# Kernel optimization log

Hardware: AMD Instinct MI355X
Metric: run time of the kernel (lower is better)

The kernel has to match this reference:

```python
import jax, jax.numpy as jnp
import numpy as np

B, S, D, HD = 4, 4096, 1024, 64

def setup_inputs() -> dict:
    key = jax.random.key(0)
    ks = jax.random.split(key, 4)
    scale = 1.0 / np.sqrt(D)
    return {
        "x": jax.random.normal(ks[0], (B, S, D), dtype=jnp.float32),
        "wq": jax.random.normal(ks[1], (HD, D), dtype=jnp.float32) * scale,
        "bq": jnp.zeros((HD,), dtype=jnp.float32),
        "wk": jax.random.normal(ks[2], (HD, D), dtype=jnp.float32) * scale,
        "bk": jnp.zeros((HD,), dtype=jnp.float32),
        "wv": jax.random.normal(ks[3], (HD, D), dtype=jnp.float32) * scale,
        "bv": jnp.zeros((HD,), dtype=jnp.float32),
    }

def reference(x, wq, bq, wk, bk, wv, bv):
    seq_len = x.shape[1]
    head_dim = wq.shape[0]
    # projections: nn.Linear stores weight as [out, in]
    q = jnp.einsum('bsd,hd->bsh', x, wq) + bq  # [B,S,HD]
    k = jnp.einsum('bsd,hd->bsh', x, wk) + bk
    v = jnp.einsum('bsd,hd->bsh', x, wv) + bv
    score = jnp.einsum('bqh,bkh->bqk', q, k) / jnp.sqrt(jnp.float32(head_dim))  # [B,S,S]
    causal = jnp.tril(jnp.ones((seq_len, seq_len), dtype=bool))
    score = jnp.where(causal, score, -jnp.inf)
    attn = jax.nn.softmax(score, axis=-1)
    # dropout p=0.0 -> identity
    out = jnp.einsum('bqk,bkh->bqh', attn, v)  # [B,S,HD]
    return out
```

## Files before the change

### kernel.cpp

```cpp
#include <hip/hip_runtime.h>
#include <math.h>

#define B_   4
#define S_   4096
#define D_   1024
#define HD_  64

#define CK            8
#define CHUNKS_PER_B  288
#define PSTRIDE       68
#define SLOT_F        (64 * PSTRIDE)

typedef float  f32x4  __attribute__((ext_vector_type(4)));
typedef __bf16 bf16x8 __attribute__((ext_vector_type(8)));

static __device__ __forceinline__ unsigned short f2bf(float f) {
    unsigned int u = __float_as_uint(f);
    u += 0x7FFFu + ((u >> 16) & 1u);
    return (unsigned short)(u >> 16);
}

__global__ __launch_bounds__(256) void convert_w(
    const float* __restrict__ wq, const float* __restrict__ wk,
    const float* __restrict__ wv, unsigned short* __restrict__ wbf)
{
    const int col = blockIdx.x;
    const int p = col >> 6, h = col & 63;
    const float* src = (p == 0 ? wq : (p == 1 ? wk : wv)) + (size_t)h * D_;
    const int t = threadIdx.x;
    const float4 v = ((const float4*)src)[t];
    ushort4 o;
    o.x = f2bf(v.x); o.y = f2bf(v.y); o.z = f2bf(v.z); o.w = f2bf(v.w);
    *(ushort4*)&wbf[(size_t)col * D_ + 4 * t] = o;
}

__global__ __launch_bounds__(256) void proj_mfma(
    const float* __restrict__ x, const unsigned short* __restrict__ wbf,
    const float* __restrict__ bq, const float* __restrict__ bk,
    const float* __restrict__ bv,
    unsigned short* __restrict__ qbf, unsigned short* __restrict__ kbf,
    unsigned short* __restrict__ vtb)
{
    __shared__ unsigned short xs[32][72];
    __shared__ unsigned short wsh[96][72];

    const int t = threadIdx.x;
    const int w = t >> 6, lane = t & 63;
    const int n = lane & 15, g = lane >> 4;
    const int koff = 8 * g;
    const int rt = w & 1, cg = w >> 1;
    const size_t row0 = (size_t)blockIdx.x * 32;
    const int colbase = 96 * blockIdx.y;

    f32x4 acc[3];
#pragma unroll
    for (int i = 0; i < 3; ++i) acc[i] = (f32x4)0.f;

    for (int chunk = 0; chunk < 16; ++chunk) {
        const int d0 = chunk * 64;
        __syncthreads();
#pragma unroll
        for (int i = 0; i < 2; ++i) {
            int e = t + i * 256;
            int r = e >> 4, c4 = (e & 15) * 4;
            float4 v = *(const float4*)&x[(row0 + r) * D_ + d0 + c4];
            ushort4 o;
            o.x = f2bf(v.x); o.y = f2bf(v.y); o.z = f2bf(v.z); o.w = f2bf(v.w);
            *(ushort4*)&xs[r][c4] = o;
        }
#pragma unroll
        for (int i = 0; i < 3; ++i) {
            int e = t + i * 256;
            int col = e >> 3, gg = e & 7;
            uint4 v = *(const uint4*)&wbf[(size_t)(colbase + col) * D_ + d0 + 8 * gg];
            *(uint4*)&wsh[col][8 * gg] = v;
        }
        __syncthreads();

#pragma unroll
        for (int ks = 0; ks < 2; ++ks) {
            const int k0 = 32 * ks;
            const bf16x8 a = *(const bf16x8*)&xs[16 * rt + n][k0 + koff];
#pragma unroll
            for (int ci = 0; ci < 3; ++ci) {
                const bf16x8 b = *(const bf16x8*)&wsh[48 * cg + 16 * ci + n][k0 + koff];
                acc[ci] = __builtin_amdgcn_mfma_f32_16x16x32_bf16(a, b, acc[ci], 0, 0, 0);
            }
        }
    }

#pragma unroll
    for (int ci = 0; ci < 3; ++ci) {
        const int gct = 6 * blockIdx.y + 3 * cg + ci;
        const int p = gct >> 2, h0 = (gct & 3) * 16;
        const int h = h0 + n;
        const float bb = (p == 0 ? bq : (p == 1 ? bk : bv))[h];
        if (p == 2) {
            const size_t grow0 = row0 + 16 * rt + 4 * g;
            const int bidx = (int)(grow0 >> 12);
            const int s0 = (int)(grow0 & 4095);
            ushort4 u;
            u.x = f2bf(acc[ci][0] + bb); u.y = f2bf(acc[ci][1] + bb);
            u.z = f2bf(acc[ci][2] + bb); u.w = f2bf(acc[ci][3] + bb);
            *(ushort4*)&vtb[((size_t)bidx * HD_ + h) * S_ + s0] = u;
        } else {
            unsigned short* outp = (p == 0 ? qbf : kbf);
            const float scale = (p == 0) ? 0.125f : 1.0f;
#pragma unroll
            for (int r = 0; r < 4; ++r) {
                const size_t grow = row0 + 16 * rt + 4 * g + r;
                outp[grow * HD_ + h] = f2bf((acc[ci][r] + bb) * scale);
            }
        }
    }
}

__global__ __launch_bounds__(256) void flash_splitk(
    const unsigned short* __restrict__ qg, const unsigned short* __restrict__ kg,
    const unsigned short* __restrict__ vt, float* __restrict__ out,
    float* __restrict__ part)
{
    __shared__ unsigned short qsh[64][72];
    __shared__ unsigned short ksh[64][72];
    __shared__ unsigned short vsh[64][72];
    __shared__ unsigned short psh[4][16][72];

    const int t    = threadIdx.x;
    const int w    = t >> 6;
    const int lane = t & 63;
    const int n    = lane & 15;
    const int g    = lane >> 4;
    const int koff = 8 * g;
    const int b    = blockIdx.y;

    int qi = 0, rem = blockIdx.x;
    while (rem >= ((qi >> 3) + 1)) { rem -= (qi >> 3) + 1; ++qi; }
    const int c   = rem;
    const int kt0 = c * CK;
    const int kt1 = min(qi, kt0 + CK - 1);
    const int nc  = (qi >> 3) + 1;

    const size_t qtile = ((size_t)b * S_ + (size_t)qi * 64) * HD_;

    {
        const uint4* src = (const uint4*)(qg + qtile);
#pragma unroll
        for (int i = 0; i < 2; ++i) {
            int e = t + i * 256;
            int r = e >> 3, gg = e & 7;
            *(uint4*)&qsh[r][8 * gg] = src[e];
        }
    }

    f32x4 o4[4];
#pragma unroll
    for (int i = 0; i < 4; ++i) o4[i] = (f32x4)0.f;
    float m_r = -INFINITY, l_r = 0.f;

    for (int kt = kt0; kt <= kt1; ++kt) {
        const size_t kvbase = ((size_t)b * S_ + (size_t)kt * 64) * HD_;
        __syncthreads();
        {
            const uint4* ksrc = (const uint4*)(kg + kvbase);
#pragma unroll
            for (int i = 0; i < 2; ++i) {
                int e = t + i * 256;
                int r = e >> 3, gg = e & 7;
                *(uint4*)&ksh[r][8 * gg] = ksrc[e];
            }
#pragma unroll
            for (int i = 0; i < 2; ++i) {
                int e = t + i * 256;
                int h = e >> 3, gg = e & 7;
                *(uint4*)&vsh[h][8 * gg] =
                    *(const uint4*)&vt[((size_t)b * HD_ + h) * S_ + kt * 64 + 8 * gg];
            }
        }
        __syncthreads();

        f32x4 sc[4];
#pragma unroll
        for (int mt = 0; mt < 4; ++mt) sc[mt] = (f32x4)0.f;
#pragma unroll
        for (int ks = 0; ks < 2; ++ks) {
            const bf16x8 bq8 = *(const bf16x8*)&qsh[16 * w + n][32 * ks + koff];
#pragma unroll
            for (int mt = 0; mt < 4; ++mt) {
                const bf16x8 ak = *(const bf16x8*)&ksh[16 * mt + n][32 * ks + koff];
                sc[mt] = __builtin_amdgcn_mfma_f32_16x16x32_bf16(ak, bq8, sc[mt], 0, 0, 0);
            }
        }

        if (kt == qi) {
            const int qloc = 16 * w + n;
#pragma unroll
            for (int mt = 0; mt < 4; ++mt)
#pragma unroll
                for (int r = 0; r < 4; ++r) {
                    const int kloc = 16 * mt + 4 * g + r;
                    if (kloc > qloc) sc[mt][r] = -INFINITY;
                }
        }

        float mx = -INFINITY;
#pragma unroll
        for (int mt = 0; mt < 4; ++mt)
#pragma unroll
            for (int r = 0; r < 4; ++r) mx = fmaxf(mx, sc[mt][r]);
        mx = fmaxf(mx, __shfl_xor(mx, 16));
        mx = fmaxf(mx, __shfl_xor(mx, 32));

        const float m_new = fmaxf(m_r, mx);
        const float alpha = __expf(m_r - m_new);
        float psum = 0.f;
#pragma unroll
        for (int mt = 0; mt < 4; ++mt)
#pragma unroll
            for (int r = 0; r < 4; ++r) {
                const float p = __expf(sc[mt][r] - m_new);
                sc[mt][r] = p;
                psum += p;
            }
        psum += __shfl_xor(psum, 16);
        psum += __shfl_xor(psum, 32);
        l_r = l_r * alpha + psum;
        m_r = m_new;

#pragma unroll
        for (int r = 0; r < 4; ++r) {
            const float ar = __shfl(alpha, 4 * g + r);
#pragma unroll
            for (int ht = 0; ht < 4; ++ht) o4[ht][r] *= ar;
        }

#pragma unroll
        for (int mt = 0; mt < 4; ++mt) {
            ushort4 u;
            u.x = f2bf(sc[mt][0]); u.y = f2bf(sc[mt][1]);
            u.z = f2bf(sc[mt][2]); u.w = f2bf(sc[mt][3]);
            *(ushort4*)&psh[w][n][16 * mt + 4 * g] = u;
        }

#pragma unroll
        for (int ks = 0; ks < 2; ++ks) {
            const bf16x8 ap = *(const bf16x8*)&psh[w][n][32 * ks + koff];
#pragma unroll
            for (int ht = 0; ht < 4; ++ht) {
                const bf16x8 bv8 = *(const bf16x8*)&vsh[16 * ht + n][32 * ks + koff];
                o4[ht] = __builtin_amdgcn_mfma_f32_16x16x32_bf16(ap, bv8, o4[ht], 0, 0, 0);
            }
        }
    }

    const size_t qbase = ((size_t)b * S_ + (size_t)qi * 64) * HD_;
    if (nc == 1) {
#pragma unroll
        for (int r = 0; r < 4; ++r) {
            const float lr = __shfl(l_r, 4 * g + r);
            const float inv = 1.f / lr;
            const size_t ob = qbase + (size_t)(16 * w + 4 * g + r) * HD_;
#pragma unroll
            for (int ht = 0; ht < 4; ++ht)
                out[ob + 16 * ht + n] = o4[ht][r] * inv;
        }
    } else {
        const size_t sb = ((size_t)b * CHUNKS_PER_B + blockIdx.x) * SLOT_F;
#pragma unroll
        for (int r = 0; r < 4; ++r) {
            const size_t pb = sb + (size_t)(16 * w + 4 * g + r) * PSTRIDE;
#pragma unroll
            for (int ht = 0; ht < 4; ++ht)
                part[pb + 16 * ht + n] = o4[ht][r];
        }
        if (g == 0) {
            part[sb + (size_t)(16 * w + n) * PSTRIDE + 64] = m_r;
            part[sb + (size_t)(16 * w + n) * PSTRIDE + 65] = l_r;
        }
    }
}

__global__ __launch_bounds__(256) void combine(
    const float* __restrict__ part, float* __restrict__ out)
{
    const int t  = threadIdx.x;
    const int qr = t >> 2, tc = t & 3;
    const int qi = blockIdx.x + CK;
    const int b  = blockIdx.y;
    const int nc = (qi >> 3) + 1;

    int cum = 0;
    for (int j = 0; j < qi; ++j) cum += (j >> 3) + 1;
    const size_t base0 = ((size_t)b * CHUNKS_PER_B + cum) * SLOT_F;

    float M = -INFINITY;
    for (int c0 = 0; c0 < nc; ++c0)
        M = fmaxf(M, part[base0 + (size_t)c0 * SLOT_F + qr * PSTRIDE + 64]);

    float L = 0.f;
    float o[16];
#pragma unroll
    for (int j = 0; j < 16; ++j) o[j] = 0.f;

    for (int c0 = 0; c0 < nc; ++c0) {
        const size_t sb = base0 + (size_t)c0 * SLOT_F + qr * PSTRIDE;
        const float m_c = part[sb + 64];
        const float l_c = part[sb + 65];
        const float w = __expf(m_c - M);
        L += w * l_c;
#pragma unroll
        for (int j = 0; j < 4; ++j) {
            const float4 ov = *(const float4*)&part[sb + tc * 16 + 4 * j];
            o[4 * j + 0] += w * ov.x; o[4 * j + 1] += w * ov.y;
            o[4 * j + 2] += w * ov.z; o[4 * j + 3] += w * ov.w;
        }
    }

    const float inv = 1.f / L;
    const size_t qbase = ((size_t)b * S_ + (size_t)qi * 64) * HD_;
#pragma unroll
    for (int j = 0; j < 4; ++j) {
        float4 r;
        r.x = o[4 * j + 0] * inv; r.y = o[4 * j + 1] * inv;
        r.z = o[4 * j + 2] * inv; r.w = o[4 * j + 3] * inv;
        *(float4*)&out[qbase + 16 * t + 4 * j] = r;
    }
}

extern "C" void kernel_launch(void* const* d_in, const int* in_sizes, int n_in,
                              void* d_out, int out_size, void* d_ws, size_t ws_size,
                              hipStream_t stream)
{
    const float* x  = (const float*)d_in[0];
    const float* wq = (const float*)d_in[1];
    const float* bq = (const float*)d_in[2];
    const float* wk = (const float*)d_in[3];
    const float* bk = (const float*)d_in[4];
    const float* wv = (const float*)d_in[5];
    const float* bv = (const float*)d_in[6];
    float* outp = (float*)d_out;

    const size_t n = (size_t)B_ * S_ * HD_;
    unsigned short* qbf = (unsigned short*)d_ws;
    unsigned short* kbf = qbf + n;
    unsigned short* vtb = kbf + n;
    unsigned short* wbf = vtb + n;
    float* part = (float*)(wbf + (size_t)192 * D_);

    convert_w<<<dim3(192), 256, 0, stream>>>(wq, wk, wv, wbf);
    proj_mfma<<<dim3(B_ * S_ / 32, 2), 256, 0, stream>>>(
        x, wbf, bq, bk, bv, qbf, kbf, vtb);
    flash_splitk<<<dim3(CHUNKS_PER_B, B_), 256, 0, stream>>>(qbf, kbf, vtb, outp, part);
    combine<<<dim3(S_ / 64 - CK, B_), 256, 0, stream>>>(part, outp);
}
```

Baseline: 174.0 us.

## Prefetch next tiles into registers in projection and attention loops

The projection kernel now double-buffers its shared-memory tiles of x and weights and loads the next chunk from global memory into registers while MFMAs run on the current one, so each chunk needs one barrier instead of two. The attention kernel likewise prefetches the next K/V tile into registers before computing on the current tile, which lets global-load latency overlap with compute. This costs extra registers and doubles the projection kernel's LDS use, which could lower occupancy.

Result: slower. 221.3 us (+27.2%).

```diff
diff --git a/kernel.cpp b/kernel.cpp
--- a/kernel.cpp
+++ b/kernel.cpp
@@ -41,8 +41,8 @@
     unsigned short* __restrict__ qbf, unsigned short* __restrict__ kbf,
     unsigned short* __restrict__ vtb)
 {
-    __shared__ unsigned short xs[32][72];
-    __shared__ unsigned short wsh[96][72];
+    __shared__ unsigned short xs[2][32][72];
+    __shared__ unsigned short wsh[2][96][72];
 
     const int t = threadIdx.x;
     const int w = t >> 6, lane = t & 63;
@@ -52,41 +52,60 @@
     const size_t row0 = (size_t)blockIdx.x * 32;
     const int colbase = 96 * blockIdx.y;
 
+    const int xr0 = t >> 4, xc4 = (t & 15) * 4;
+    const int wc0 = t >> 3, wg8 = (t & 7) * 8;
+
+    float4 xr[2];
+    uint4  wr[3];
+
+    auto loadXW = [&](int chunk) {
+        const int d0 = chunk * 64;
+#pragma unroll
+        for (int i = 0; i < 2; ++i)
+            xr[i] = *(const float4*)&x[(row0 + xr0 + 16 * i) * D_ + d0 + xc4];
+#pragma unroll
+        for (int i = 0; i < 3; ++i)
+            wr[i] = *(const uint4*)&wbf[(size_t)(colbase + wc0 + 32 * i) * D_ + d0 + wg8];
+    };
+    auto storeXW = [&](int buf) {
+#pragma unroll
+        for (int i = 0; i < 2; ++i) {
+            ushort4 o;
+            o.x = f2bf(xr[i].x); o.y = f2bf(xr[i].y);
+            o.z = f2bf(xr[i].z); o.w = f2bf(xr[i].w);
+            *(ushort4*)&xs[buf][xr0 + 16 * i][xc4] = o;
+        }
+#pragma unroll
+        for (int i = 0; i < 3; ++i)
+            *(uint4*)&wsh[buf][wc0 + 32 * i][wg8] = wr[i];
+    };
+
     f32x4 acc[3];
 #pragma unroll
     for (int i = 0; i < 3; ++i) acc[i] = (f32x4)0.f;
 
-    for (int chunk = 0; chunk < 16; ++chunk) {
-        const int d0 = chunk * 64;
-        __syncthreads();
-#pragma unroll
-        for (int i = 0; i < 2; ++i) {
-            int e = t + i * 256;
-            int r = e >> 4, c4 = (e & 15) * 4;
-            float4 v = *(const float4*)&x[(row0 + r) * D_ + d0 + c4];
-            ushort4 o;
-            o.x = f2bf(v.x); o.y = f2bf(v.y); o.z = f2bf(v.z); o.w = f2bf(v.w);
-            *(ushort4*)&xs[r][c4] = o;
-        }
-#pragma unroll
-        for (int i = 0; i < 3; ++i) {
-            int e = t + i * 256;
-            int col = e >> 3, gg = e & 7;
-            uint4 v = *(const uint4*)&wbf[(size_t)(colbase + col) * D_ + d0 + 8 * gg];
-            *(uint4*)&wsh[col][8 * gg] = v;
-        }
-        __syncthreads();
-
+    loadXW(0);
+    storeXW(0);
+    loadXW(1);
+    __syncthreads();
+
+    for (int c = 0; c < 16; ++c) {
+        const int cur = c & 1;
 #pragma unroll
         for (int ks = 0; ks < 2; ++ks) {
             const int k0 = 32 * ks;
-            const bf16x8 a = *(const bf16x8*)&xs[16 * rt + n][k0 + koff];
+            const bf16x8 a = *(const bf16x8*)&xs[cur][16 * rt + n][k0 + koff];
 #pragma unroll
             for (int ci = 0; ci < 3; ++ci) {
-                const bf16x8 b = *(const bf16x8*)&wsh[48 * cg + 16 * ci + n][k0 + koff];
+                const bf16x8 b = *(const bf16x8*)&wsh[cur][48 * cg + 16 * ci + n][k0 + koff];
                 acc[ci] = __builtin_amdgcn_mfma_f32_16x16x32_bf16(a, b, acc[ci], 0, 0, 0);
             }
         }
+        if (c < 15) {
+            storeXW(1 - cur);
+            if (c < 14) loadXW(c + 2);
+        }
+        __syncthreads();
     }
 
 #pragma unroll
@@ -142,6 +161,8 @@
 
     const size_t qtile = ((size_t)b * S_ + (size_t)qi * 64) * HD_;
 
+    const int sr = t >> 3, sg8 = (t & 7) * 8;
+
     {
         const uint4* src = (const uint4*)(qg + qtile);
 #pragma unroll
@@ -152,30 +173,34 @@
         }
     }
 
+    uint4 kr[2], vr[2];
+    auto loadKV = [&](int kt) {
+        const size_t kvbase = ((size_t)b * S_ + (size_t)kt * 64) * HD_;
+#pragma unroll
+        for (int i = 0; i < 2; ++i)
+            kr[i] = *(const uint4*)&kg[kvbase + (size_t)(sr + 32 * i) * HD_ + sg8];
+#pragma unroll
+        for (int i = 0; i < 2; ++i)
+            vr[i] = *(const uint4*)&vt[((size_t)b * HD_ + (sr + 32 * i)) * S_ + kt * 64 + sg8];
+    };
+    auto storeKV = [&]() {
+#pragma unroll
+        for (int i = 0; i < 2; ++i) *(uint4*)&ksh[sr + 32 * i][sg8] = kr[i];
+#pragma unroll
+        for (int i = 0; i < 2; ++i) *(uint4*)&vsh[sr + 32 * i][sg8] = vr[i];
+    };
+
     f32x4 o4[4];
 #pragma unroll
     for (int i = 0; i < 4; ++i) o4[i] = (f32x4)0.f;
     float m_r = -INFINITY, l_r = 0.f;
 
+    loadKV(kt0);
+
     for (int kt = kt0; kt <= kt1; ++kt) {
-        const size_t kvbase = ((size_t)b * S_ + (size_t)kt * 64) * HD_;
         __syncthreads();
-        {
-            const uint4* ksrc = (const uint4*)(kg + kvbase);
-#pragma unroll
-            for (int i = 0; i < 2; ++i) {
-                int e = t + i * 256;
-                int r = e >> 3, gg = e & 7;
-                *(uint4*)&ksh[r][8 * gg] = ksrc[e];
-            }
-#pragma unroll
-            for (int i = 0; i < 2; ++i) {
-                int e = t + i * 256;
-                int h = e >> 3, gg = e & 7;
-                *(uint4*)&vsh[h][8 * gg] =
-                    *(const uint4*)&vt[((size_t)b * HD_ + h) * S_ + kt * 64 + 8 * gg];
-            }
-        }
+        storeKV();
+        if (kt < kt1) loadKV(kt + 1);
         __syncthreads();
 
         f32x4 sc[4];
```
